# Kernel tuning notes

Measured on AMD Instinct MI355X. Metric: run time of the kernel, lower is better.

The kernel has to match this reference:

```python
import jax, jax.numpy as jnp
import numpy as np

B, P, N, E, H, KD, M = 64, 100, 1000, 512, 8, 64, 10
SQRT_E = float(np.sqrt(E))
CLIP = 10.0


def _heads(x):
    # [b, n, H*KD] -> [b, H, n, KD]
    b, n, _ = x.shape
    return x.reshape(b, n, H, KD).transpose(0, 2, 1, 3)


def setup_inputs() -> dict:
    key = jax.random.key(0)
    ks = jax.random.split(key, 20)
    f = jnp.float32
    s = 0.02  # weight init scale
    return {
        "encoded_last_node": jax.random.normal(ks[0], (B, P, E), f),
        "encoded_last_agents": jax.random.normal(ks[1], (B, P, E), f),
        "cur_dist": jax.random.uniform(ks[2], (B, P, N), f, 1e-3, 1.0),
        "ninf_mask": jnp.zeros((B, P, N), f),
        "lengths": jax.random.uniform(ks[3], (B, P, M), f),
        "max_dis": jax.random.uniform(ks[4], (B, P, 1), f),
        "remain_max_dis": jax.random.uniform(ks[5], (B, P, 1), f),
        "q_first": 0.5 * jax.random.normal(ks[6], (B, H, P, KD), f),
        "k": 0.5 * jax.random.normal(ks[7], (B, H, N, KD), f),
        "v": 0.5 * jax.random.normal(ks[8], (B, H, N, KD), f),
        "single_head_key": 0.5 * jax.random.normal(ks[9], (B, E, N), f),
        "Wq_last_w": s * jax.random.normal(ks[10], (H * KD, 2 * E + 2), f),
        "dis_emb_w": s * jax.random.normal(ks[11], (H * KD, 4), f),
        "mh_w": s * jax.random.normal(ks[12], (E, H * KD), f),
        "mh_b": s * jax.random.normal(ks[13], (E,), f),
        "dist_alpha": jnp.ones((1,), f),
        "depot_num": jax.random.randint(ks[14], (B,), 1, M + 1),
        "route_cnt": jax.random.randint(ks[15], (B, P, 1), 0, M),
        "left_city": jax.random.randint(ks[16], (B, P), 0, N + 1),
        "city_num": N,
    }


def reference(encoded_last_node, encoded_last_agents, cur_dist, ninf_mask,
              lengths, max_dis, remain_max_dis, q_first, k, v, single_head_key,
              Wq_last_w, dis_emb_w, mh_w, mh_b, dist_alpha,
              depot_num, route_cnt, left_city, city_num):
    # route_num = depot_num - 1, broadcast to route_cnt shape [B,P,1]
    route_num = jnp.broadcast_to(depot_num[:, None, None], route_cnt.shape) - 1
    g_cur = jnp.take_along_axis(lengths, route_cnt, axis=-1)    # [B,P,1]
    g_route = jnp.take_along_axis(lengths, route_num, axis=-1)  # [B,P,1]
    q_info_in = jnp.concatenate([g_cur, g_route, max_dis, remain_max_dis], axis=-1)  # [B,P,4]
    q_info = _heads(q_info_in @ dis_emb_w.T)  # [B,H,P,KD]

    frac = 1.0 - (route_cnt + 1).astype(jnp.float32) / (route_num + 1).astype(jnp.float32)
    lc = left_city[:, :, None].astype(jnp.float32) / city_num
    q_last_in = jnp.concatenate([encoded_last_node, encoded_last_agents, frac, lc], axis=-1)  # [B,P,2E+2]
    q_last = _heads(q_last_in @ Wq_last_w.T)  # [B,H,P,KD]

    q = q_first + q_last + q_info  # [B,H,P,KD]

    # masked multi-head attention (rank3 ninf mask)
    score = jnp.einsum("bhpd,bhnd->bhpn", q, k) / jnp.sqrt(jnp.float32(KD))
    score = score + ninf_mask[:, None, :, :]
    w = jax.nn.softmax(score, axis=-1)
    out = jnp.einsum("bhpn,bhnd->bhpd", w, v)
    out_concat = out.transpose(0, 2, 1, 3).reshape(out.shape[0], out.shape[2], H * KD)  # [B,P,H*KD]
    mh = out_concat @ mh_w.T + mh_b  # [B,P,E]

    # single-head distance-biased scoring
    score2 = jnp.einsum("bpe,ben->bpn", mh, single_head_key)  # [B,P,N]
    max_dist = jnp.max(cur_dist, axis=-1, keepdims=True)
    cur_dist_out = -cur_dist / max_dist
    score_clipped = CLIP * jnp.tanh(score2 / SQRT_E + dist_alpha * cur_dist_out)
    probs = jax.nn.softmax(score_clipped + ninf_mask, axis=-1)
    return probs
```

## Files before the change

kernel.cpp:

```cpp
#include <hip/hip_runtime.h>
#include <hip/hip_bf16.h>

#define BB 64
#define PP 100
#define NN 1000
#define EE 512
#define HH 8
#define KDD 64
#define MM 10
#define ROWS (BB*PP)
#define K1K 1026
#define INVSQE 0.044194173824159216f
#define CLIPV 10.0f

union F4 { float4 v; float f[4]; };

using bf16x8 = __attribute__((ext_vector_type(8))) short;
using f32x4  = __attribute__((ext_vector_type(4))) float;

__device__ inline unsigned short f2bf(float x) {
  unsigned u = __float_as_uint(x);
  u += 0x7FFFu + ((u >> 16) & 1u);
  return (unsigned short)(u >> 16);
}

__device__ inline float bf2f(unsigned short s) {
  return __uint_as_float(((unsigned)s) << 16);
}

__device__ inline float fast_tanh(float x) {
  float e = __expf(2.0f * x);
  return 1.0f - 2.0f / (e + 1.0f);
}

__global__ __launch_bounds__(256) void k_rowmax(const float* __restrict__ cd,
                                                float* __restrict__ rmax) {
  int row = blockIdx.x * 4 + (threadIdx.x >> 6);
  int lane = threadIdx.x & 63;
  const float* src = cd + (size_t)row * NN;
  float m = -1e30f;
  for (int i = lane; i < NN; i += 64) m = fmaxf(m, src[i]);
  #pragma unroll
  for (int off = 32; off; off >>= 1) m = fmaxf(m, __shfl_xor(m, off));
  if (lane == 0) rmax[row] = m;
}

__global__ __launch_bounds__(256) void k_qgemm(
    const float* __restrict__ eln, const float* __restrict__ ela,
    const float* __restrict__ lengths, const float* __restrict__ max_dis,
    const float* __restrict__ remain, const float* __restrict__ q_first,
    const float* __restrict__ Wq, const float* __restrict__ dis_emb,
    const int* __restrict__ depot, const int* __restrict__ route_cnt,
    const int* __restrict__ left_city, const int* __restrict__ city_num,
    float* __restrict__ qout) {
  __shared__ unsigned short Xs[64][40];
  __shared__ unsigned short Ws[64][40];
  __shared__ float info_s[64][4];
  __shared__ float fl_s[64][2];
  const int t = threadIdx.x;
  const int lane = t & 63;
  const int w = t >> 6;
  const int lr = lane & 15, lg = lane >> 4;
  const int rowBase = blockIdx.y * 64, colBase = blockIdx.x * 64;

  if (t < 64) {
    int row = rowBase + t;
    int b = row / PP;
    int rc = route_cnt[row];
    int rn = depot[b] - 1;
    info_s[t][0] = lengths[row * MM + rc];
    info_s[t][1] = lengths[row * MM + rn];
    info_s[t][2] = max_dis[row];
    info_s[t][3] = remain[row];
    fl_s[t][0] = 1.0f - (float)(rc + 1) / (float)(rn + 1);
    fl_s[t][1] = (float)left_city[row] / (float)city_num[0];
  }

  f32x4 acc[4];
  #pragma unroll
  for (int m = 0; m < 4; ++m) { acc[m][0] = 0.f; acc[m][1] = 0.f; acc[m][2] = 0.f; acc[m][3] = 0.f; }

  for (int kt = 0; kt < 32; ++kt) {
    const float* xsrc = (kt < 16) ? eln : ela;
    const int koff = (kt & 15) * 32;
    __syncthreads();
    #pragma unroll
    for (int i = 0; i < 2; ++i) {
      int s = i * 256 + t;
      int r = s >> 3, c4 = (s & 7) * 4;
      F4 xv, wv;
      xv.v = *(const float4*)&xsrc[(size_t)(rowBase + r) * 512 + koff + c4];
      wv.v = *(const float4*)&Wq[(size_t)(colBase + r) * K1K + kt * 32 + c4];
      unsigned short* xd = &Xs[r][c4];
      unsigned short* wd = &Ws[r][c4];
      xd[0] = f2bf(xv.f[0]); xd[1] = f2bf(xv.f[1]); xd[2] = f2bf(xv.f[2]); xd[3] = f2bf(xv.f[3]);
      wd[0] = f2bf(wv.f[0]); wd[1] = f2bf(wv.f[1]); wd[2] = f2bf(wv.f[2]); wd[3] = f2bf(wv.f[3]);
    }
    __syncthreads();
    bf16x8 bfr = *(bf16x8*)&Ws[w * 16 + lr][lg * 8];
    #pragma unroll
    for (int m = 0; m < 4; ++m) {
      bf16x8 af = *(bf16x8*)&Xs[m * 16 + lr][lg * 8];
      acc[m] = __builtin_amdgcn_mfma_f32_16x16x32_bf16(af, bfr, acc[m], 0, 0, 0);
    }
  }

  const int o = colBase + w * 16 + lr;
  F4 de; de.v = *(const float4*)&dis_emb[(size_t)o * 4];
  const float wq1024 = Wq[(size_t)o * K1K + 1024];
  const float wq1025 = Wq[(size_t)o * K1K + 1025];
  const int h = o >> 6, kd = o & 63;
  #pragma unroll
  for (int m = 0; m < 4; ++m) {
    #pragma unroll
    for (int j = 0; j < 4; ++j) {
      int r = m * 16 + lg * 4 + j;
      int row = rowBase + r;
      int b = row / PP, p = row % PP;
      F4 inf; inf.v = *(const float4*)&info_s[r][0];
      float v = acc[m][j]
              + inf.f[0] * de.f[0] + inf.f[1] * de.f[1]
              + inf.f[2] * de.f[2] + inf.f[3] * de.f[3]
              + fl_s[r][0] * wq1024 + fl_s[r][1] * wq1025
              + q_first[(((size_t)b * HH + h) * PP + p) * KDD + kd];
      qout[(size_t)row * 512 + o] = v;
    }
  }
}

__global__ __launch_bounds__(256) void k_attn(
    const float* __restrict__ qin, const float* __restrict__ kk,
    const float* __restrict__ vv, const float* __restrict__ mask,
    float* __restrict__ attn_out) {
  __shared__ unsigned short Kl[64][72];
  __shared__ unsigned short Vt[64][72];
  __shared__ unsigned short PMb[64][72];

  const int t = threadIdx.x;
  const int lane = t & 63;
  const int w = t >> 6;
  const int lr = lane & 15, lg = lane >> 4;
  const int gid = blockIdx.x;
  const int b = gid & 63;
  const int X = gid >> 6;
  const int h = X & 7, half = X >> 3;
  const int bh = b * HH + h;
  const int p0 = half * 64;
  const int nrows = (half == 0) ? 64 : (PP - 64);
  const bool active = (w * 16 < nrows);

  #pragma unroll
  for (int i = 0; i < 4; ++i) {
    int idx = i * 256 + t;
    int r = idx >> 4, c4 = (idx & 15) * 4;
    int p = p0 + r;
    F4 qv; qv.v = make_float4(0.f, 0.f, 0.f, 0.f);
    if (p < PP) qv.v = *(const float4*)&qin[((size_t)(b * PP + p)) * 512 + h * 64 + c4];
    unsigned short* d = &PMb[r][c4];
    d[0] = f2bf(qv.f[0] * 0.125f); d[1] = f2bf(qv.f[1] * 0.125f);
    d[2] = f2bf(qv.f[2] * 0.125f); d[3] = f2bf(qv.f[3] * 0.125f);
  }
  __syncthreads();

  bf16x8 qf[2];
  qf[0] = *(bf16x8*)&PMb[w * 16 + lr][lg * 8];
  qf[1] = *(bf16x8*)&PMb[w * 16 + lr][32 + lg * 8];
  __syncthreads();

  float Lacc[4] = {0.f, 0.f, 0.f, 0.f};
  f32x4 Oa[4];
  #pragma unroll
  for (int dt = 0; dt < 4; ++dt) { Oa[dt][0] = 0.f; Oa[dt][1] = 0.f; Oa[dt][2] = 0.f; Oa[dt][3] = 0.f; }

  for (int ch = 0; ch < 16; ++ch) {
    const int n0 = ch * 64;

    #pragma unroll
    for (int i = 0; i < 4; ++i) {
      int idx = i * 256 + t;
      int r = idx >> 4, c4 = (idx & 15) * 4;
      int n = n0 + r;
      F4 kv; kv.v = make_float4(0.f, 0.f, 0.f, 0.f);
      if (n < NN) kv.v = *(const float4*)&kk[(((size_t)bh * NN) + n) * 64 + c4];
      unsigned short* d = &Kl[r][c4];
      d[0] = f2bf(kv.f[0]); d[1] = f2bf(kv.f[1]); d[2] = f2bf(kv.f[2]); d[3] = f2bf(kv.f[3]);
    }
    {
      int b2 = t & 15, a = t >> 4;
      F4 rowv[4];
      #pragma unroll
      for (int r = 0; r < 4; ++r) {
        int n = n0 + 4 * b2 + r;
        rowv[r].v = (n < NN) ? *(const float4*)&vv[(((size_t)bh * NN) + n) * 64 + 4 * a]
                             : make_float4(0.f, 0.f, 0.f, 0.f);
      }
      #pragma unroll
      for (int c = 0; c < 4; ++c) {
        unsigned short* dst = &Vt[4 * a + c][4 * b2];
        dst[0] = f2bf(rowv[0].f[c]); dst[1] = f2bf(rowv[1].f[c]);
        dst[2] = f2bf(rowv[2].f[c]); dst[3] = f2bf(rowv[3].f[c]);
      }
    }
    #pragma unroll
    for (int i = 0; i < 4; ++i) {
      int idx = i * 256 + t;
      int r = idx >> 4, c4 = (idx & 15) * 4;
      if (r < nrows) {
        int p = p0 + r, n = n0 + c4;
        F4 mv;
        if (n + 3 < NN) {
          mv.v = *(const float4*)&mask[((size_t)(b * PP + p)) * NN + n];
        } else {
          #pragma unroll
          for (int j = 0; j < 4; ++j)
            mv.f[j] = (n + j < NN) ? mask[((size_t)(b * PP + p)) * NN + n + j] : -1e30f;
        }
        unsigned short* d = &PMb[r][c4];
        d[0] = f2bf(mv.f[0]); d[1] = f2bf(mv.f[1]); d[2] = f2bf(mv.f[2]); d[3] = f2bf(mv.f[3]);
      }
    }
    __syncthreads();

    if (active) {
      f32x4 sa[4];
      #pragma unroll
      for (int nb = 0; nb < 4; ++nb) { sa[nb][0] = 0.f; sa[nb][1] = 0.f; sa[nb][2] = 0.f; sa[nb][3] = 0.f; }
      #pragma unroll
      for (int kb = 0; kb < 2; ++kb)
        #pragma unroll
        for (int nb = 0; nb < 4; ++nb) {
          bf16x8 kf = *(bf16x8*)&Kl[nb * 16 + lr][kb * 32 + lg * 8];
          sa[nb] = __builtin_amdgcn_mfma_f32_16x16x32_bf16(qf[kb], kf, sa[nb], 0, 0, 0);
        }
      #pragma unroll
      for (int j = 0; j < 4; ++j) {
        int pr = w * 16 + lg * 4 + j;
        #pragma unroll
        for (int nb = 0; nb < 4; ++nb) {
          float mv = bf2f(PMb[pr][nb * 16 + lr]);
          float e = __expf(sa[nb][j] + mv);
          Lacc[j] += e;
          PMb[pr][nb * 16 + lr] = f2bf(e);
        }
      }
      #pragma unroll
      for (int kb = 0; kb < 2; ++kb) {
        bf16x8 pf = *(bf16x8*)&PMb[w * 16 + lr][kb * 32 + lg * 8];
        #pragma unroll
        for (int dt = 0; dt < 4; ++dt) {
          bf16x8 vf = *(bf16x8*)&Vt[dt * 16 + lr][kb * 32 + lg * 8];
          Oa[dt] = __builtin_amdgcn_mfma_f32_16x16x32_bf16(pf, vf, Oa[dt], 0, 0, 0);
        }
      }
    }
    __syncthreads();
  }

  if (active) {
    #pragma unroll
    for (int j = 0; j < 4; ++j) {
      float L = Lacc[j];
      #pragma unroll
      for (int off = 1; off < 16; off <<= 1) L += __shfl_xor(L, off);
      int p = p0 + w * 16 + lg * 4 + j;
      if (p < PP) {
        float inv = (L > 0.f) ? 1.0f / L : 0.f;
        #pragma unroll
        for (int dt = 0; dt < 4; ++dt)
          attn_out[((size_t)(b * PP + p)) * 512 + h * 64 + dt * 16 + lr] = Oa[dt][j] * inv;
      }
    }
  }
}

__global__ __launch_bounds__(256) void k_mhgemm(
    const float* __restrict__ A, const float* __restrict__ W,
    const float* __restrict__ bias, float* __restrict__ out) {
  __shared__ unsigned short Xs[64][40];
  __shared__ unsigned short Ws[64][40];
  const int t = threadIdx.x;
  const int lane = t & 63;
  const int w = t >> 6;
  const int lr = lane & 15, lg = lane >> 4;
  const int rowBase = blockIdx.y * 64, colBase = blockIdx.x * 64;

  f32x4 acc[4];
  #pragma unroll
  for (int m = 0; m < 4; ++m) { acc[m][0] = 0.f; acc[m][1] = 0.f; acc[m][2] = 0.f; acc[m][3] = 0.f; }

  for (int kt = 0; kt < 16; ++kt) {
    const int koff = kt * 32;
    __syncthreads();
    #pragma unroll
    for (int i = 0; i < 2; ++i) {
      int s = i * 256 + t;
      int r = s >> 3, c4 = (s & 7) * 4;
      F4 xv, wv;
      xv.v = *(const float4*)&A[(size_t)(rowBase + r) * 512 + koff + c4];
      wv.v = *(const float4*)&W[(size_t)(colBase + r) * 512 + koff + c4];
      unsigned short* xd = &Xs[r][c4];
      unsigned short* wd = &Ws[r][c4];
      xd[0] = f2bf(xv.f[0]); xd[1] = f2bf(xv.f[1]); xd[2] = f2bf(xv.f[2]); xd[3] = f2bf(xv.f[3]);
      wd[0] = f2bf(wv.f[0]); wd[1] = f2bf(wv.f[1]); wd[2] = f2bf(wv.f[2]); wd[3] = f2bf(wv.f[3]);
    }
    __syncthreads();
    bf16x8 bfr = *(bf16x8*)&Ws[w * 16 + lr][lg * 8];
    #pragma unroll
    for (int m = 0; m < 4; ++m) {
      bf16x8 af = *(bf16x8*)&Xs[m * 16 + lr][lg * 8];
      acc[m] = __builtin_amdgcn_mfma_f32_16x16x32_bf16(af, bfr, acc[m], 0, 0, 0);
    }
  }

  const int o = colBase + w * 16 + lr;
  const float bv = bias[o];
  #pragma unroll
  for (int m = 0; m < 4; ++m) {
    #pragma unroll
    for (int j = 0; j < 4; ++j) {
      int row = rowBase + m * 16 + lg * 4 + j;
      out[(size_t)row * 512 + o] = acc[m][j] + bv;
    }
  }
}

__global__ __launch_bounds__(256) void k_final_score(
    const float* __restrict__ mh, const float* __restrict__ shk,
    const float* __restrict__ cur_dist, const float* __restrict__ rmax,
    const float* __restrict__ mask, const float* __restrict__ dist_alpha,
    float* __restrict__ sc_out) {
  __shared__ unsigned short As[112][40];
  __shared__ unsigned short Bt[64][40];
  const int t = threadIdx.x;
  const int lane = t & 63;
  const int w = t >> 6;
  const int lr = lane & 15, lg = lane >> 4;
  const int n0 = blockIdx.x * 64, b = blockIdx.y;

  f32x4 acc[7];
  #pragma unroll
  for (int m = 0; m < 7; ++m) { acc[m][0] = 0.f; acc[m][1] = 0.f; acc[m][2] = 0.f; acc[m][3] = 0.f; }

  for (int kt = 0; kt < 16; ++kt) {
    const int k0 = kt * 32;
    __syncthreads();
    #pragma unroll
    for (int i = 0; i < 4; ++i) {
      int s = i * 256 + t;
      if (s < 896) {
        int r = s >> 3, c4 = (s & 7) * 4;
        F4 xv; xv.v = make_float4(0.f, 0.f, 0.f, 0.f);
        if (r < PP) xv.v = *(const float4*)&mh[(size_t)(b * PP + r) * 512 + k0 + c4];
        unsigned short* xd = &As[r][c4];
        xd[0] = f2bf(xv.f[0]); xd[1] = f2bf(xv.f[1]); xd[2] = f2bf(xv.f[2]); xd[3] = f2bf(xv.f[3]);
      }
    }
    if (t < 128) {
      int a = t & 15, kb = t >> 4;
      F4 rowv[4];
      #pragma unroll
      for (int r = 0; r < 4; ++r) {
        int k = k0 + 4 * kb + r;
        int n = n0 + 4 * a;
        rowv[r].v = (n < NN) ? *(const float4*)&shk[((size_t)b * EE + k) * NN + n]
                             : make_float4(0.f, 0.f, 0.f, 0.f);
      }
      #pragma unroll
      for (int c = 0; c < 4; ++c) {
        unsigned short* dst = &Bt[4 * a + c][4 * kb];
        dst[0] = f2bf(rowv[0].f[c]); dst[1] = f2bf(rowv[1].f[c]);
        dst[2] = f2bf(rowv[2].f[c]); dst[3] = f2bf(rowv[3].f[c]);
      }
    }
    __syncthreads();
    bf16x8 bfr = *(bf16x8*)&Bt[w * 16 + lr][lg * 8];
    #pragma unroll
    for (int m = 0; m < 7; ++m) {
      bf16x8 af = *(bf16x8*)&As[m * 16 + lr][lg * 8];
      acc[m] = __builtin_amdgcn_mfma_f32_16x16x32_bf16(af, bfr, acc[m], 0, 0, 0);
    }
  }

  const float alpha = dist_alpha[0];
  const int n = n0 + w * 16 + lr;
  if (n < NN) {
    #pragma unroll
    for (int m = 0; m < 7; ++m) {
      #pragma unroll
      for (int j = 0; j < 4; ++j) {
        int p = m * 16 + lg * 4 + j;
        if (p >= PP) continue;
        size_t rb = (size_t)(b * PP + p) * NN;
        float rmx = rmax[b * PP + p];
        float cd = cur_dist[rb + n];
        float mk = mask[rb + n];
        sc_out[rb + n] = CLIPV * fast_tanh(acc[m][j] * INVSQE - alpha * cd / rmx) + mk;
      }
    }
  }
}

__global__ __launch_bounds__(256) void k_softmax(const float* __restrict__ sc,
                                                 float* __restrict__ out) {
  __shared__ float redm[4];
  __shared__ float redsum[4];
  const int row = blockIdx.x;
  const int t = threadIdx.x;
  const float* src = sc + (size_t)row * NN;
  float v0[4];
  float m = -1e30f;
  #pragma unroll
  for (int i = 0; i < 4; ++i) {
    int n = i * 256 + t;
    v0[i] = (n < NN) ? src[n] : -1e30f;
    m = fmaxf(m, v0[i]);
  }
  #pragma unroll
  for (int off = 32; off; off >>= 1) m = fmaxf(m, __shfl_xor(m, off));
  int wid = t >> 6, lane = t & 63;
  if (lane == 0) redm[wid] = m;
  __syncthreads();
  m = fmaxf(fmaxf(redm[0], redm[1]), fmaxf(redm[2], redm[3]));
  float e[4];
  float s = 0.f;
  #pragma unroll
  for (int i = 0; i < 4; ++i) {
    int n = i * 256 + t;
    e[i] = (n < NN) ? __expf(v0[i] - m) : 0.f;
    s += e[i];
  }
  #pragma unroll
  for (int off = 32; off; off >>= 1) s += __shfl_xor(s, off);
  if (lane == 0) redsum[wid] = s;
  __syncthreads();
  s = redsum[0] + redsum[1] + redsum[2] + redsum[3];
  float inv = 1.0f / s;
  #pragma unroll
  for (int i = 0; i < 4; ++i) {
    int n = i * 256 + t;
    if (n < NN) out[(size_t)row * NN + n] = e[i] * inv;
  }
}

extern "C" void kernel_launch(void* const* d_in, const int* in_sizes, int n_in,
                              void* d_out, int out_size, void* d_ws, size_t ws_size,
                              hipStream_t stream) {
  const float* eln       = (const float*)d_in[0];
  const float* ela       = (const float*)d_in[1];
  const float* cur_dist  = (const float*)d_in[2];
  const float* ninf      = (const float*)d_in[3];
  const float* lengths   = (const float*)d_in[4];
  const float* max_dis   = (const float*)d_in[5];
  const float* remain    = (const float*)d_in[6];
  const float* q_first   = (const float*)d_in[7];
  const float* kten      = (const float*)d_in[8];
  const float* vten      = (const float*)d_in[9];
  const float* shk       = (const float*)d_in[10];
  const float* Wq        = (const float*)d_in[11];
  const float* dis_emb   = (const float*)d_in[12];
  const float* mh_w      = (const float*)d_in[13];
  const float* mh_b      = (const float*)d_in[14];
  const float* dalpha    = (const float*)d_in[15];
  const int*   depot     = (const int*)d_in[16];
  const int*   route_cnt = (const int*)d_in[17];
  const int*   left_city = (const int*)d_in[18];
  const int*   city_num  = (const int*)d_in[19];
  float* out = (float*)d_out;

  float* ws      = (float*)d_ws;
  float* q_ws    = ws;
  float* attn_ws = q_ws + (size_t)ROWS * 512;
  float* mh_ws   = attn_ws + (size_t)ROWS * 512;
  float* sc_ws   = mh_ws + (size_t)ROWS * 512;
  float* rmax_ws = sc_ws + (size_t)ROWS * NN;

  k_rowmax<<<ROWS / 4, 256, 0, stream>>>(cur_dist, rmax_ws);
  k_qgemm<<<dim3(8, 100), 256, 0, stream>>>(eln, ela, lengths, max_dis, remain,
                                            q_first, Wq, dis_emb, depot, route_cnt,
                                            left_city, city_num, q_ws);
  k_attn<<<1024, 256, 0, stream>>>(q_ws, kten, vten, ninf, attn_ws);
  k_mhgemm<<<dim3(8, 100), 256, 0, stream>>>(attn_ws, mh_w, mh_b, mh_ws);
  k_final_score<<<dim3(16, 64), 256, 0, stream>>>(mh_ws, shk, cur_dist, rmax_ws,
                                                  ninf, dalpha, sc_ws);
  k_softmax<<<ROWS, 256, 0, stream>>>(sc_ws, out);
}
```

Baseline: 288.9 us.

## Prefetch next K/V chunk into registers and load mask directly per lane

The attention kernel now loads the next chunk of K and V from global memory into registers while the current chunk is computed, so global load latency overlaps with the MFMA work. The mask is read straight from global memory into registers in the MFMA output layout instead of being staged through shared memory as bf16. Shared-memory stores are packed into 4-wide vectors, and the sync points are rearranged so there are two per chunk. The cost is higher register pressure and uncoalesced per-lane mask reads. The mask now also stays in fp32 rather than being rounded to bf16.

```diff
diff --git a/kernel.cpp b/kernel.cpp
--- a/kernel.cpp
+++ b/kernel.cpp
@@ -16,6 +16,7 @@
 union F4 { float4 v; float f[4]; };
 
 using bf16x8 = __attribute__((ext_vector_type(8))) short;
+using bf16x4 = __attribute__((ext_vector_type(4))) unsigned short;
 using f32x4  = __attribute__((ext_vector_type(4))) float;
 
 __device__ inline unsigned short f2bf(float x) {
@@ -134,7 +135,7 @@
     float* __restrict__ attn_out) {
   __shared__ unsigned short Kl[64][72];
   __shared__ unsigned short Vt[64][72];
-  __shared__ unsigned short PMb[64][72];
+  __shared__ unsigned short Pb[64][72];
 
   const int t = threadIdx.x;
   const int lane = t & 63;
@@ -156,72 +157,90 @@
     int p = p0 + r;
     F4 qv; qv.v = make_float4(0.f, 0.f, 0.f, 0.f);
     if (p < PP) qv.v = *(const float4*)&qin[((size_t)(b * PP + p)) * 512 + h * 64 + c4];
-    unsigned short* d = &PMb[r][c4];
-    d[0] = f2bf(qv.f[0] * 0.125f); d[1] = f2bf(qv.f[1] * 0.125f);
-    d[2] = f2bf(qv.f[2] * 0.125f); d[3] = f2bf(qv.f[3] * 0.125f);
+    bf16x4 pk;
+    pk[0] = f2bf(qv.f[0] * 0.125f); pk[1] = f2bf(qv.f[1] * 0.125f);
+    pk[2] = f2bf(qv.f[2] * 0.125f); pk[3] = f2bf(qv.f[3] * 0.125f);
+    *(bf16x4*)&Pb[r][c4] = pk;
   }
   __syncthreads();
 
   bf16x8 qf[2];
-  qf[0] = *(bf16x8*)&PMb[w * 16 + lr][lg * 8];
-  qf[1] = *(bf16x8*)&PMb[w * 16 + lr][32 + lg * 8];
-  __syncthreads();
+  qf[0] = *(bf16x8*)&Pb[w * 16 + lr][lg * 8];
+  qf[1] = *(bf16x8*)&Pb[w * 16 + lr][32 + lg * 8];
 
   float Lacc[4] = {0.f, 0.f, 0.f, 0.f};
   f32x4 Oa[4];
   #pragma unroll
   for (int dt = 0; dt < 4; ++dt) { Oa[dt][0] = 0.f; Oa[dt][1] = 0.f; Oa[dt][2] = 0.f; Oa[dt][3] = 0.f; }
 
+  F4 kreg[4], vreg[4];
+  const int vb2 = t & 15, va = t >> 4;
+
+  #pragma unroll
+  for (int i = 0; i < 4; ++i) {
+    int idx = i * 256 + t;
+    int r = idx >> 4, c4 = (idx & 15) * 4;
+    kreg[i].v = (r < NN) ? *(const float4*)&kk[(((size_t)bh * NN) + r) * 64 + c4]
+                         : make_float4(0.f, 0.f, 0.f, 0.f);
+  }
+  #pragma unroll
+  for (int r = 0; r < 4; ++r) {
+    int n = 4 * vb2 + r;
+    vreg[r].v = (n < NN) ? *(const float4*)&vv[(((size_t)bh * NN) + n) * 64 + 4 * va]
+                         : make_float4(0.f, 0.f, 0.f, 0.f);
+  }
+
   for (int ch = 0; ch < 16; ++ch) {
     const int n0 = ch * 64;
+    __syncthreads();
 
     #pragma unroll
     for (int i = 0; i < 4; ++i) {
       int idx = i * 256 + t;
       int r = idx >> 4, c4 = (idx & 15) * 4;
-      int n = n0 + r;
-      F4 kv; kv.v = make_float4(0.f, 0.f, 0.f, 0.f);
-      if (n < NN) kv.v = *(const float4*)&kk[(((size_t)bh * NN) + n) * 64 + c4];
-      unsigned short* d = &Kl[r][c4];
-      d[0] = f2bf(kv.f[0]); d[1] = f2bf(kv.f[1]); d[2] = f2bf(kv.f[2]); d[3] = f2bf(kv.f[3]);
-    }
-    {
-      int b2 = t & 15, a = t >> 4;
-      F4 rowv[4];
+      bf16x4 pk;
+      pk[0] = f2bf(kreg[i].f[0]); pk[1] = f2bf(kreg[i].f[1]);
+      pk[2] = f2bf(kreg[i].f[2]); pk[3] = f2bf(kreg[i].f[3]);
+      *(bf16x4*)&Kl[r][c4] = pk;
+    }
+    #pragma unroll
+    for (int c = 0; c < 4; ++c) {
+      bf16x4 pv;
+      pv[0] = f2bf(vreg[0].f[c]); pv[1] = f2bf(vreg[1].f[c]);
+      pv[2] = f2bf(vreg[2].f[c]); pv[3] = f2bf(vreg[3].f[c]);
+      *(bf16x4*)&Vt[4 * va + c][4 * vb2] = pv;
+    }
+    __syncthreads();
+
+    if (ch + 1 < 16) {
+      const int nn0 = n0 + 64;
+      #pragma unroll
+      for (int i = 0; i < 4; ++i) {
+        int idx = i * 256 + t;
+        int r = idx >> 4, c4 = (idx & 15) * 4;
+        int n = nn0 + r;
+        kreg[i].v = (n < NN) ? *(const float4*)&kk[(((size_t)bh * NN) + n) * 64 + c4]
+                             : make_float4(0.f, 0.f, 0.f, 0.f);
+      }
       #pragma unroll
       for (int r = 0; r < 4; ++r) {
-        int n = n0 + 4 * b2 + r;
-        rowv[r].v = (n < NN) ? *(const float4*)&vv[(((size_t)bh * NN) + n) * 64 + 4 * a]
+        int n = nn0 + 4 * vb2 + r;
+        vreg[r].v = (n < NN) ? *(const float4*)&vv[(((size_t)bh * NN) + n) * 64 + 4 * va]
                              : make_float4(0.f, 0.f, 0.f, 0.f);
       }
-      #pragma unroll
-      for (int c = 0; c < 4; ++c) {
-        unsigned short* dst = &Vt[4 * a + c][4 * b2];
-        dst[0] = f2bf(rowv[0].f[c]); dst[1] = f2bf(rowv[1].f[c]);
-        dst[2] = f2bf(rowv[2].f[c]); dst[3] = f2bf(rowv[3].f[c]);
-      }
-    }
-    #pragma unroll
-    for (int i = 0; i < 4; ++i) {
-      int idx = i * 256 + t;
-      int r = idx >> 4, c4 = (idx & 15) * 4;
-      if (r < nrows) {
-        int p = p0 + r, n = n0 + c4;
-        F4 mv;
-        if (n + 3 < NN) {
-          mv.v = *(const float4*)&mask[((size_t)(b * PP + p)) * NN + n];
-        } else {
-          #pragma unroll
-          for (int j = 0; j < 4; ++j)
-            mv.f[j] = (n + j < NN) ? mask[((size_t)(b * PP + p)) * NN + n + j] : -1e30f;
+    }
+
+    if (active) {
+      float ml[4][4];
+      #pragma unroll
+      for (int j = 0; j < 4; ++j) {
+        int p = p0 + w * 16 + lg * 4 + j;
+        #pragma unroll
+        for (int nb = 0; nb < 4; ++nb) {
+          int n = n0 + nb * 16 + lr;
+          ml[j][nb] = (p < PP && n < NN) ? mask[((size_t)(b * PP + p)) * NN + n] : -1e30f;
         }
-        unsigned short* d = &PMb[r][c4];
-        d[0] = f2bf(mv.f[0]); d[1] = f2bf(mv.f[1]); d[2] = f2bf(mv.f[2]); d[3] = f2bf(mv.f[3]);
-      }
-    }
-    __syncthreads();
-
-    if (active) {
+      }
       f32x4 sa[4];
       #pragma unroll
       for (int nb = 0; nb < 4; ++nb) { sa[nb][0] = 0.f; sa[nb][1] = 0.f; sa[nb][2] = 0.f; sa[nb][3] = 0.f; }
@@ -237,15 +256,14 @@
         int pr = w * 16 + lg * 4 + j;
         #pragma unroll
         for (int nb = 0; nb < 4; ++nb) {
-          float mv = bf2f(PMb[pr][nb * 16 + lr]);
-          float e = __expf(sa[nb][j] + mv);
+          float e = __expf(sa[nb][j] + ml[j][nb]);
           Lacc[j] += e;
-          PMb[pr][nb * 16 + lr] = f2bf(e);
+          Pb[pr][nb * 16 + lr] = f2bf(e);
         }
       }
       #pragma unroll
       for (int kb = 0; kb < 2; ++kb) {
-        bf16x8 pf = *(bf16x8*)&PMb[w * 16 + lr][kb * 32 + lg * 8];
+        bf16x8 pf = *(bf16x8*)&Pb[w * 16 + lr][kb * 32 + lg * 8];
         #pragma unroll
         for (int dt = 0; dt < 4; ++dt) {
           bf16x8 vf = *(bf16x8*)&Vt[dt * 16 + lr][kb * 32 + lg * 8];
@@ -253,7 +271,6 @@
         }
       }
     }
-    __syncthreads();
   }
 
   if (active) {
```

After: 285.4 us. Within noise of the previous version (-1.2%).
